# Kernel optimization log

Measured on AMD Instinct MI355X. Metric: run time of the kernel, lower is better.

## Reference

```python
import jax, jax.numpy as jnp
import numpy as np


def _gcn_conv(x, W, b, src, dst, n_nodes):
    """PyG-style GCNConv: XW, symmetric deg^-1/2 normalization over edges
    (with self-loops already included in src/dst), scatter-add to targets, + bias."""
    xw = x @ W  # [N, F_out]
    ones = jnp.ones(src.shape[0], dtype=xw.dtype)
    deg = jax.ops.segment_sum(ones, dst, num_segments=n_nodes)  # in-degree incl. self-loops
    dinv = jnp.where(deg > 0, jax.lax.rsqrt(jnp.maximum(deg, 1.0)), 0.0)
    norm = dinv[src] * dinv[dst]                        # [E]
    msgs = xw[src] * norm[:, None]                      # [E, F_out] gather + scale
    out = jax.ops.segment_sum(msgs, dst, num_segments=n_nodes)  # scatter-add
    return out + b


def setup_inputs() -> dict:
    key = jax.random.key(0)
    k1, k2, k3, k4 = jax.random.split(key, 4)
    N, E = 100000, 1600000
    IN, HID, OUT = 128, 64, 64
    x = jax.random.normal(k1, (N, IN), dtype=jnp.float32)
    edge_index = jax.random.randint(k2, (2, E), 0, N, dtype=jnp.int64)
    W1 = jax.random.normal(k3, (IN, HID), dtype=jnp.float32) * (1.0 / np.sqrt(IN))
    b1 = jnp.zeros((HID,), dtype=jnp.float32)
    W2 = jax.random.normal(k4, (HID, OUT), dtype=jnp.float32) * (1.0 / np.sqrt(HID))
    b2 = jnp.zeros((OUT,), dtype=jnp.float32)
    return {"x": x, "edge_index": edge_index, "W1": W1, "b1": b1, "W2": W2, "b2": b2}


def reference(x, edge_index, W1, b1, W2, b2):
    n_nodes = x.shape[0]
    # add self-loops (PyG GCNConv default add_self_loops=True)
    loops = jnp.arange(n_nodes, dtype=edge_index.dtype)
    src = jnp.concatenate([edge_index[0], loops])
    dst = jnp.concatenate([edge_index[1], loops])
    h = _gcn_conv(x, W1, b1, src, dst, n_nodes)
    h = jax.nn.relu(h)
    z = _gcn_conv(h, W2, b2, src, dst, n_nodes)
    return z
```

## Files before the change

kernel.cpp:

```cpp
#include <hip/hip_runtime.h>

#define IN_F 128
#define HID_F 64
#define BKT_SHIFT 9
#define BKT_SIZE 512
#define CHUNK 4096

typedef unsigned short ushort_t;
typedef __attribute__((ext_vector_type(8))) short bf16x8;
typedef __attribute__((ext_vector_type(8))) unsigned short u16x8;
typedef __attribute__((ext_vector_type(4))) float f32x4;

__device__ inline ushort_t f2bf(float f) {
    unsigned u = __float_as_uint(f);
    u += 0x7FFFu + ((u >> 16) & 1u);
    return (ushort_t)(u >> 16);
}
__device__ inline float bf2f(ushort_t u) {
    return __uint_as_float((unsigned)u << 16);
}


__global__ __launch_bounds__(256) void k_hist(const int* __restrict__ dst,
        int* __restrict__ ghist, int E) {
    __shared__ int hist[256];
    int tid = threadIdx.x;
    hist[tid] = 0;
    __syncthreads();
    int e0 = blockIdx.x * CHUNK, e1 = min(e0 + CHUNK, E);
    for (int e = e0 + tid; e < e1; e += 256)
        atomicAdd(&hist[dst[e] >> BKT_SHIFT], 1);
    __syncthreads();
    ghist[blockIdx.x * 256 + tid] = hist[tid];
}

__global__ __launch_bounds__(256) void k_colscan(int* __restrict__ ghist,
        int* __restrict__ gcount, int nb) {
    __shared__ int s[256];
    int t = threadIdx.x;
    int b = blockIdx.x;
    int j0 = 2 * t, j1 = 2 * t + 1;
    int v0 = (j0 < nb) ? ghist[j0 * 256 + b] : 0;
    int v1 = (j1 < nb) ? ghist[j1 * 256 + b] : 0;
    int p = v0 + v1;
    s[t] = p;
    __syncthreads();
    for (int off = 1; off < 256; off <<= 1) {
        int v = (t >= off) ? s[t - off] : 0;
        __syncthreads();
        s[t] += v;
        __syncthreads();
    }
    int excl = s[t] - p;
    if (j0 < nb) ghist[j0 * 256 + b] = excl;
    if (j1 < nb) ghist[j1 * 256 + b] = excl + v0;
    if (t == 255) gcount[b] = s[255];
}

__global__ __launch_bounds__(256) void k_bscan(const int* __restrict__ gcount,
        int* __restrict__ gbase, int* __restrict__ bbase,
        int* __restrict__ rowptr, int N, int E) {
    __shared__ int s[256];
    int t = threadIdx.x;
    int c = gcount[t];
    s[t] = c;
    __syncthreads();
    for (int off = 1; off < 256; off <<= 1) {
        int v = (t >= off) ? s[t - off] : 0;
        __syncthreads();
        s[t] += v;
        __syncthreads();
    }
    int base = s[t] - c;
    gbase[t] = base;
    bbase[t] = base;
    if (t == 255) bbase[256] = s[255];
    if (t == 0) rowptr[N] = E;
}

__global__ __launch_bounds__(256) void k_scatter(const int* __restrict__ src,
        const int* __restrict__ dst, const int* __restrict__ ghist,
        const int* __restrict__ gbase, unsigned* __restrict__ gbin, int E) {
    __shared__ int cur[256];
    int tid = threadIdx.x;
    cur[tid] = ghist[blockIdx.x * 256 + tid] + gbase[tid];
    __syncthreads();
    int e0 = blockIdx.x * CHUNK, e1 = min(e0 + CHUNK, E);
    for (int e = e0 + tid; e < e1; e += 256) {
        int d = dst[e];
        int b = d >> BKT_SHIFT;
        int p = atomicAdd(&cur[b], 1);
        gbin[p] = ((unsigned)(d & (BKT_SIZE - 1)) << 23) | (unsigned)src[e];
    }
}

__global__ __launch_bounds__(256) void k_fill2(const unsigned* __restrict__ gbin,
        const int* __restrict__ bbase, int* __restrict__ rowptr,
        float* __restrict__ dinv, int* __restrict__ col, int N) {
    __shared__ int cnt[BKT_SIZE];
    __shared__ int pos[BKT_SIZE];
    __shared__ int s[256];
    int tid = threadIdx.x;
    int b = blockIdx.x;
    int e0 = bbase[b], e1 = bbase[b + 1];
    cnt[tid] = 0; cnt[tid + 256] = 0;
    __syncthreads();
    for (int e = e0 + tid; e < e1; e += 256)
        atomicAdd(&cnt[gbin[e] >> 23], 1);
    __syncthreads();
    int c0 = cnt[2 * tid], c1 = cnt[2 * tid + 1];
    int p2 = c0 + c1;
    s[tid] = p2;
    __syncthreads();
    for (int off = 1; off < 256; off <<= 1) {
        int v = (tid >= off) ? s[tid - off] : 0;
        __syncthreads();
        s[tid] += v;
        __syncthreads();
    }
    int excl = s[tid] - p2;
    pos[2 * tid] = excl;
    pos[2 * tid + 1] = excl + c0;
    __syncthreads();
    int n0 = b << BKT_SHIFT;
    #pragma unroll
    for (int i = tid; i < BKT_SIZE; i += 256) {
        int n = n0 + i;
        if (n < N) {
            rowptr[n] = e0 + pos[i];
            dinv[n] = rsqrtf((float)cnt[i] + 1.0f);
        }
    }
    __syncthreads();
    for (int e = e0 + tid; e < e1; e += 256) {
        unsigned v = gbin[e];
        int p = atomicAdd(&pos[v >> 23], 1);
        col[e0 + p] = (int)(v & 0x7FFFFFu);
    }
}

__global__ void k_pack(const float* __restrict__ W1, const float* __restrict__ W2,
                       ushort_t* __restrict__ Bp1, ushort_t* __restrict__ Bp2) {
    int tid = blockIdx.x * 256 + threadIdx.x;
    int id = (tid < 8192) ? tid : tid - 8192;
    int j = id & 7, lane = (id >> 3) & 63, t = (id >> 9) & 3, s = id >> 11;
    int k = s * 32 + ((lane >> 4) << 3) + j;
    int n = t * 16 + (lane & 15);
    if (tid < 8192)        Bp1[id] = f2bf(W1[k * 64 + n]);
    else if (tid < 12288)  Bp2[id] = f2bf(W2[k * 64 + n]);
}

template<int K, typename AT>
__global__ __launch_bounds__(256) void k_gemm_mfma(const AT* __restrict__ A,
        const ushort_t* __restrict__ Bp, const float* __restrict__ dinv,
        ushort_t* __restrict__ out, int N) {
    int wave = threadIdx.x >> 6, lane = threadIdx.x & 63;
    int m = lane & 15, q = lane >> 4;
    int row0 = blockIdx.x * 64 + wave * 16;
    int arow = row0 + m;
    int arowc = (arow < N) ? arow : (N - 1);
    f32x4 acc[4] = {};
    #pragma unroll
    for (int s = 0; s < K / 32; ++s) {
        bf16x8 af;
        if constexpr (sizeof(AT) == 4) {
            const float* ap = (const float*)A + (size_t)arowc * K + s * 32 + q * 8;
            float4 x0 = *(const float4*)ap;
            float4 x1 = *(const float4*)(ap + 4);
            af[0] = (short)f2bf(x0.x); af[1] = (short)f2bf(x0.y);
            af[2] = (short)f2bf(x0.z); af[3] = (short)f2bf(x0.w);
            af[4] = (short)f2bf(x1.x); af[5] = (short)f2bf(x1.y);
            af[6] = (short)f2bf(x1.z); af[7] = (short)f2bf(x1.w);
        } else {
            af = *(const bf16x8*)((const ushort_t*)A + (size_t)arowc * K + s * 32 + q * 8);
        }
        #pragma unroll
        for (int t = 0; t < 4; ++t) {
            bf16x8 bf = *(const bf16x8*)(Bp + (size_t)((s * 4 + t) * 64 + lane) * 8);
            acc[t] = __builtin_amdgcn_mfma_f32_16x16x32_bf16(af, bf, acc[t], 0, 0, 0);
        }
    }
    int orow0 = row0 + q * 4;
    float4 d4 = *(const float4*)(dinv + orow0);
    #pragma unroll
    for (int r = 0; r < 4; ++r) {
        int row = orow0 + r;
        if (row < N) {
            float dn = (r == 0) ? d4.x : (r == 1) ? d4.y : (r == 2) ? d4.z : d4.w;
            #pragma unroll
            for (int t = 0; t < 4; ++t)
                out[(size_t)row * 64 + t * 16 + m] = f2bf(acc[t][r] * dn);
        }
    }
}

__global__ __launch_bounds__(256) void k_aggregate(const ushort_t* __restrict__ xws,
        const int* __restrict__ rowptr, const int* __restrict__ col,
        const float* __restrict__ dinv, const float* __restrict__ bias,
        float* __restrict__ outf, ushort_t* __restrict__ outb, int N, int relu_bf16) {
    int n = (blockIdx.x * 256 + threadIdx.x) >> 3;
    int i = threadIdx.x & 7;
    if (n >= N) return;
    int beg = rowptr[n], end = rowptr[n + 1];
    float dn = dinv[n];
    const ushort_t* base = xws + i * 8;
    u16x8 sv = *(const u16x8*)(base + (size_t)n * 64);
    float a[8];
    #pragma unroll
    for (int k = 0; k < 8; ++k) a[k] = bf2f(sv[k]);
    int e = beg;
    for (; e + 8 <= end; e += 8) {
        int c[8];
        #pragma unroll
        for (int j = 0; j < 8; ++j) c[j] = col[e + j];
        u16x8 v[8];
        #pragma unroll
        for (int j = 0; j < 8; ++j) v[j] = *(const u16x8*)(base + (size_t)c[j] * 64);
        #pragma unroll
        for (int j = 0; j < 8; ++j)
            #pragma unroll
            for (int k = 0; k < 8; ++k) a[k] += bf2f(v[j][k]);
    }
    if (e + 4 <= end) {
        int c[4];
        #pragma unroll
        for (int j = 0; j < 4; ++j) c[j] = col[e + j];
        u16x8 v[4];
        #pragma unroll
        for (int j = 0; j < 4; ++j) v[j] = *(const u16x8*)(base + (size_t)c[j] * 64);
        #pragma unroll
        for (int j = 0; j < 4; ++j)
            #pragma unroll
            for (int k = 0; k < 8; ++k) a[k] += bf2f(v[j][k]);
        e += 4;
    }
    for (; e < end; ++e) {
        u16x8 v = *(const u16x8*)(base + (size_t)col[e] * 64);
        #pragma unroll
        for (int k = 0; k < 8; ++k) a[k] += bf2f(v[k]);
    }
    float4 b0 = *(const float4*)(bias + i * 8);
    float4 b1 = *(const float4*)(bias + i * 8 + 4);
    float r[8];
    r[0] = dn * a[0] + b0.x; r[1] = dn * a[1] + b0.y;
    r[2] = dn * a[2] + b0.z; r[3] = dn * a[3] + b0.w;
    r[4] = dn * a[4] + b1.x; r[5] = dn * a[5] + b1.y;
    r[6] = dn * a[6] + b1.z; r[7] = dn * a[7] + b1.w;
    if (relu_bf16) {
        u16x8 o;
        #pragma unroll
        for (int k = 0; k < 8; ++k) o[k] = f2bf(fmaxf(r[k], 0.f));
        *(u16x8*)(outb + (size_t)n * 64 + i * 8) = o;
    } else {
        float4 o0 = {r[0], r[1], r[2], r[3]};
        float4 o1 = {r[4], r[5], r[6], r[7]};
        *(float4*)(outf + (size_t)n * 64 + i * 8) = o0;
        *(float4*)(outf + (size_t)n * 64 + i * 8 + 4) = o1;
    }
}


extern "C" void kernel_launch(void* const* d_in, const int* in_sizes, int n_in,
                              void* d_out, int out_size, void* d_ws, size_t ws_size,
                              hipStream_t stream) {
    const float* x  = (const float*)d_in[0];
    const int*   ei = (const int*)d_in[1];
    const float* W1 = (const float*)d_in[2];
    const float* b1 = (const float*)d_in[3];
    const float* W2 = (const float*)d_in[4];
    const float* b2 = (const float*)d_in[5];
    float* out = (float*)d_out;

    const int N = in_sizes[0] / IN_F;
    const int E = in_sizes[1] / 2;
    const int* src = ei;
    const int* dst = ei + E;

    char* ws = (char*)d_ws;
    const size_t MB = 1u << 20;
    int*      bbase   = (int*)     (ws + 4096);
    int*      gbase   = (int*)     (ws + 8192);
    int*      gcount  = (int*)     (ws + 12288);
    ushort_t* Bp1     = (ushort_t*)(ws + 16384);
    ushort_t* Bp2     = (ushort_t*)(ws + 49152);
    int*      rowptr  = (int*)     (ws + 1 * MB);
    float*    dinv    = (float*)   (ws + 2 * MB);
    unsigned* gbin    = (unsigned*)(ws + 3 * MB);
    int*      ghist   = (int*)     (ws + 10 * MB);
    int*      col     = (int*)     (ws + 11 * MB);
    ushort_t* xws     = (ushort_t*)(ws + 20 * MB);
    ushort_t* h       = (ushort_t*)(ws + 36 * MB);

    const int nbE = (E + CHUNK - 1) / CHUNK;
    const int nbB = (N + BKT_SIZE - 1) / BKT_SIZE;
    const int nbG = (N + 63) / 64;
    const int nbA = (N * 8 + 255) / 256;

    k_pack   <<<48, 256, 0, stream>>>(W1, W2, Bp1, Bp2);
    k_hist   <<<nbE, 256, 0, stream>>>(dst, ghist, E);
    k_colscan<<<256, 256, 0, stream>>>(ghist, gcount, nbE);
    k_bscan  <<<1, 256, 0, stream>>>(gcount, gbase, bbase, rowptr, N, E);
    k_scatter<<<nbE, 256, 0, stream>>>(src, dst, ghist, gbase, gbin, E);
    k_fill2  <<<nbB, 256, 0, stream>>>(gbin, bbase, rowptr, dinv, col, N);

    k_gemm_mfma<IN_F, float>   <<<nbG, 256, 0, stream>>>(x, Bp1, dinv, xws, N);
    k_aggregate<<<nbA, 256, 0, stream>>>(xws, rowptr, col, dinv, b1, nullptr, h, N, 1);

    k_gemm_mfma<HID_F, ushort_t><<<nbG, 256, 0, stream>>>(h, Bp2, dinv, xws, N);
    k_aggregate<<<nbA, 256, 0, stream>>>(xws, rowptr, col, dinv, b2, out, nullptr, N, 0);
}
```

Baseline: 234.3 us.

## Fold weight packing and bucket scan into neighbouring kernels; double-buffer aggregate gathers

Removes the separate k_pack and k_bscan launches. Weight packing now runs inside k_hist, and every k_scatter and k_fill2 block recomputes the 256-entry bucket prefix scan redundantly. The aggregate kernel now software-pipelines its gathers of neighbour features, issuing the next 8 loads before accumulating the previous 8, and drops the 4-wide tail block. This trades two kernel launches for redundant per-block scans and more register use in the aggregate loop.

New measurement: 256.6 us. +9.5%, slower.

```diff
diff --git a/kernel.cpp b/kernel.cpp
--- a/kernel.cpp
+++ b/kernel.cpp
@@ -22,9 +22,20 @@
 
 
 __global__ __launch_bounds__(256) void k_hist(const int* __restrict__ dst,
-        int* __restrict__ ghist, int E) {
+        int* __restrict__ ghist, int E,
+        const float* __restrict__ W1, const float* __restrict__ W2,
+        ushort_t* __restrict__ Bp1, ushort_t* __restrict__ Bp2) {
+    int tid = threadIdx.x;
+    int tg = blockIdx.x * 256 + tid;
+    if (tg < 12288) {
+        int id = (tg < 8192) ? tg : tg - 8192;
+        int j = id & 7, lane = (id >> 3) & 63, t = (id >> 9) & 3, s = id >> 11;
+        int k = s * 32 + ((lane >> 4) << 3) + j;
+        int n = t * 16 + (lane & 15);
+        if (tg < 8192) Bp1[id] = f2bf(W1[k * 64 + n]);
+        else           Bp2[id] = f2bf(W2[k * 64 + n]);
+    }
     __shared__ int hist[256];
-    int tid = threadIdx.x;
     hist[tid] = 0;
     __syncthreads();
     int e0 = blockIdx.x * CHUNK, e1 = min(e0 + CHUNK, E);
@@ -57,33 +68,22 @@
     if (t == 255) gcount[b] = s[255];
 }
 
-__global__ __launch_bounds__(256) void k_bscan(const int* __restrict__ gcount,
-        int* __restrict__ gbase, int* __restrict__ bbase,
-        int* __restrict__ rowptr, int N, int E) {
-    __shared__ int s[256];
-    int t = threadIdx.x;
-    int c = gcount[t];
-    s[t] = c;
-    __syncthreads();
-    for (int off = 1; off < 256; off <<= 1) {
-        int v = (t >= off) ? s[t - off] : 0;
-        __syncthreads();
-        s[t] += v;
-        __syncthreads();
-    }
-    int base = s[t] - c;
-    gbase[t] = base;
-    bbase[t] = base;
-    if (t == 255) bbase[256] = s[255];
-    if (t == 0) rowptr[N] = E;
-}
-
 __global__ __launch_bounds__(256) void k_scatter(const int* __restrict__ src,
         const int* __restrict__ dst, const int* __restrict__ ghist,
-        const int* __restrict__ gbase, unsigned* __restrict__ gbin, int E) {
+        const int* __restrict__ gcount, unsigned* __restrict__ gbin, int E) {
+    __shared__ int s[256];
     __shared__ int cur[256];
     int tid = threadIdx.x;
-    cur[tid] = ghist[blockIdx.x * 256 + tid] + gbase[tid];
+    int c = gcount[tid];
+    s[tid] = c;
+    __syncthreads();
+    for (int off = 1; off < 256; off <<= 1) {
+        int v = (tid >= off) ? s[tid - off] : 0;
+        __syncthreads();
+        s[tid] += v;
+        __syncthreads();
+    }
+    cur[tid] = ghist[blockIdx.x * 256 + tid] + (s[tid] - c);
     __syncthreads();
     int e0 = blockIdx.x * CHUNK, e1 = min(e0 + CHUNK, E);
     for (int e = e0 + tid; e < e1; e += 256) {
@@ -95,14 +95,28 @@
 }
 
 __global__ __launch_bounds__(256) void k_fill2(const unsigned* __restrict__ gbin,
-        const int* __restrict__ bbase, int* __restrict__ rowptr,
-        float* __restrict__ dinv, int* __restrict__ col, int N) {
+        const int* __restrict__ gcount, int* __restrict__ rowptr,
+        float* __restrict__ dinv, int* __restrict__ col, int N, int E) {
     __shared__ int cnt[BKT_SIZE];
     __shared__ int pos[BKT_SIZE];
     __shared__ int s[256];
     int tid = threadIdx.x;
     int b = blockIdx.x;
-    int e0 = bbase[b], e1 = bbase[b + 1];
+    if (b == 0 && tid == 0) rowptr[N] = E;
+    int c = gcount[tid];
+    s[tid] = c;
+    __syncthreads();
+    for (int off = 1; off < 256; off <<= 1) {
+        int v = (tid >= off) ? s[tid - off] : 0;
+        __syncthreads();
+        s[tid] += v;
+        __syncthreads();
+    }
+    cnt[tid] = s[tid] - c;
+    __syncthreads();
+    int e0 = cnt[b];
+    int e1 = (b < 255) ? cnt[b + 1] : E;
+    __syncthreads();
     cnt[tid] = 0; cnt[tid + 256] = 0;
     __syncthreads();
     for (int e = e0 + tid; e < e1; e += 256)
@@ -137,17 +151,6 @@
         int p = atomicAdd(&pos[v >> 23], 1);
         col[e0 + p] = (int)(v & 0x7FFFFFu);
     }
-}
-
-__global__ void k_pack(const float* __restrict__ W1, const float* __restrict__ W2,
-                       ushort_t* __restrict__ Bp1, ushort_t* __restrict__ Bp2) {
-    int tid = blockIdx.x * 256 + threadIdx.x;
-    int id = (tid < 8192) ? tid : tid - 8192;
-    int j = id & 7, lane = (id >> 3) & 63, t = (id >> 9) & 3, s = id >> 11;
-    int k = s * 32 + ((lane >> 4) << 3) + j;
-    int n = t * 16 + (lane & 15);
-    if (tid < 8192)        Bp1[id] = f2bf(W1[k * 64 + n]);
-    else if (tid < 12288)  Bp2[id] = f2bf(W2[k * 64 + n]);
 }
 
 template<int K, typename AT>
@@ -194,6 +197,15 @@
     }
 }
 
+#define LOAD8(C, V, E0)                                               \
+    _Pragma("unroll") for (int j = 0; j < 8; ++j) C[j] = col[(E0) + j]; \
+    _Pragma("unroll") for (int j = 0; j < 8; ++j)                      \
+        V[j] = *(const u16x8*)(base + (size_t)C[j] * 64);
+
+#define ACC8(V)                                                        \
+    _Pragma("unroll") for (int j = 0; j < 8; ++j)                      \
+        _Pragma("unroll") for (int k = 0; k < 8; ++k) a[k] += bf2f(V[j][k]);
+
 __global__ __launch_bounds__(256) void k_aggregate(const ushort_t* __restrict__ xws,
         const int* __restrict__ rowptr, const int* __restrict__ col,
         const float* __restrict__ dinv, const float* __restrict__ bias,
@@ -208,31 +220,26 @@
     float a[8];
     #pragma unroll
     for (int k = 0; k < 8; ++k) a[k] = bf2f(sv[k]);
+    int nfull = (end - beg) >> 3;
     int e = beg;
-    for (; e + 8 <= end; e += 8) {
-        int c[8];
-        #pragma unroll
-        for (int j = 0; j < 8; ++j) c[j] = col[e + j];
-        u16x8 v[8];
-        #pragma unroll
-        for (int j = 0; j < 8; ++j) v[j] = *(const u16x8*)(base + (size_t)c[j] * 64);
-        #pragma unroll
-        for (int j = 0; j < 8; ++j)
-            #pragma unroll
-            for (int k = 0; k < 8; ++k) a[k] += bf2f(v[j][k]);
-    }
-    if (e + 4 <= end) {
-        int c[4];
-        #pragma unroll
-        for (int j = 0; j < 4; ++j) c[j] = col[e + j];
-        u16x8 v[4];
-        #pragma unroll
-        for (int j = 0; j < 4; ++j) v[j] = *(const u16x8*)(base + (size_t)c[j] * 64);
-        #pragma unroll
-        for (int j = 0; j < 4; ++j)
-            #pragma unroll
-            for (int k = 0; k < 8; ++k) a[k] += bf2f(v[j][k]);
-        e += 4;
+    if (nfull > 0) {
+        int cA[8], cB[8];
+        u16x8 vA[8], vB[8];
+        LOAD8(cA, vA, e); e += 8;
+        int it = 1;
+        for (; it + 1 < nfull; it += 2) {
+            LOAD8(cB, vB, e); e += 8;
+            ACC8(vA);
+            LOAD8(cA, vA, e); e += 8;
+            ACC8(vB);
+        }
+        if (it < nfull) {
+            LOAD8(cB, vB, e); e += 8;
+            ACC8(vA);
+            ACC8(vB);
+        } else {
+            ACC8(vA);
+        }
     }
     for (; e < end; ++e) {
         u16x8 v = *(const u16x8*)(base + (size_t)col[e] * 64);
@@ -278,8 +285,6 @@
 
     char* ws = (char*)d_ws;
     const size_t MB = 1u << 20;
-    int*      bbase   = (int*)     (ws + 4096);
-    int*      gbase   = (int*)     (ws + 8192);
     int*      gcount  = (int*)     (ws + 12288);
     ushort_t* Bp1     = (ushort_t*)(ws + 16384);
     ushort_t* Bp2     = (ushort_t*)(ws + 49152);
@@ -296,12 +301,10 @@
     const int nbG = (N + 63) / 64;
     const int nbA = (N * 8 + 255) / 256;
 
-    k_pack   <<<48, 256, 0, stream>>>(W1, W2, Bp1, Bp2);
-    k_hist   <<<nbE, 256, 0, stream>>>(dst, ghist, E);
+    k_hist   <<<nbE, 256, 0, stream>>>(dst, ghist, E, W1, W2, Bp1, Bp2);
     k_colscan<<<256, 256, 0, stream>>>(ghist, gcount, nbE);
-    k_bscan  <<<1, 256, 0, stream>>>(gcount, gbase, bbase, rowptr, N, E);
-    k_scatter<<<nbE, 256, 0, stream>>>(src, dst, ghist, gbase, gbin, E);
-    k_fill2  <<<nbB, 256, 0, stream>>>(gbin, bbase, rowptr, dinv, col, N);
+    k_scatter<<<nbE, 256, 0, stream>>>(src, dst, ghist, gcount, gbin, E);
+    k_fill2  <<<nbB, 256, 0, stream>>>(gbin, gcount, rowptr, dinv, col, N, E);
 
     k_gemm_mfma<IN_F, float>   <<<nbG, 256, 0, stream>>>(x, Bp1, dinv, xws, N);
     k_aggregate<<<nbA, 256, 0, stream>>>(xws, rowptr, col, dinv, b1, nullptr, h, N, 1);
```
